# Kernel optimization log

Measured on AMD Instinct MI355X. Metric: run time of the kernel, lower is better.

Reference implementation:

```python
import jax, jax.numpy as jnp
import numpy as np

NUM_HEADS = 6
HEAD_SIZE = 64
N_EMBD = 384


def setup_inputs() -> dict:
    key = jax.random.key(0)
    ks = jax.random.split(key, 6)
    B, T, C = 4, 2048, N_EMBD
    D = NUM_HEADS * HEAD_SIZE  # 384
    x = jax.random.normal(ks[0], (B, T, C), dtype=jnp.float32)
    scale = 1.0 / np.sqrt(C)
    Wq = jax.random.normal(ks[1], (C, D), dtype=jnp.float32) * scale
    Wk = jax.random.normal(ks[2], (C, D), dtype=jnp.float32) * scale
    Wv = jax.random.normal(ks[3], (C, D), dtype=jnp.float32) * scale
    Wp = jax.random.normal(ks[4], (D, N_EMBD), dtype=jnp.float32) * scale
    bp = jnp.zeros((N_EMBD,), dtype=jnp.float32)
    return {"x": x, "Wq": Wq, "Wk": Wk, "Wv": Wv, "Wp": Wp, "bp": bp}


def reference(x, Wq, Wk, Wv, Wp, bp):
    B, T, C = x.shape
    H, Dh = NUM_HEADS, HEAD_SIZE
    # QKV projections (no bias), split into heads: [B, H, T, Dh]
    q = (x @ Wq).reshape(B, T, H, Dh).transpose(0, 2, 1, 3)
    k = (x @ Wk).reshape(B, T, H, Dh).transpose(0, 2, 1, 3)
    v = (x @ Wv).reshape(B, T, H, Dh).transpose(0, 2, 1, 3)
    # scaled dot-product scores [B, H, T, T]
    scores = jnp.einsum("bhqd,bhkd->bhqk", q, k) / jnp.sqrt(jnp.float32(Dh))
    causal = jnp.tril(jnp.ones((T, T), dtype=bool))
    scores = jnp.where(causal, scores, jnp.float32(-1e9))
    attn = jax.nn.softmax(scores, axis=-1)
    # dropout is identity at inference (Keras Dropout inactive outside training)
    out = jnp.einsum("bhqk,bhkd->bhqd", attn, v)
    out = out.transpose(0, 2, 1, 3).reshape(B, T, H * Dh)
    return out @ Wp + bp
```

## Files before the change

### kernel.cpp

```cpp
#include <hip/hip_runtime.h>
#include <hip/hip_bf16.h>

typedef __bf16 bf16x8 __attribute__((ext_vector_type(8)));
typedef float floatx4 __attribute__((ext_vector_type(4)));
typedef unsigned short us4 __attribute__((ext_vector_type(4)));
typedef unsigned short us8 __attribute__((ext_vector_type(8)));
typedef unsigned short ushort_t;

#define MFMA(a,b,c) __builtin_amdgcn_mfma_f32_16x16x32_bf16((a),(b),(c),0,0,0)


__device__ __forceinline__ ushort_t f2bf(float f){
  unsigned u = __builtin_bit_cast(unsigned, f);
  u = u + 0x7fffu + ((u>>16)&1u);
  return (ushort_t)(u>>16);
}

__device__ __forceinline__ us4 pack4(float4 a){
  us4 o;
  o[0]=f2bf(a.x); o[1]=f2bf(a.y); o[2]=f2bf(a.z); o[3]=f2bf(a.w);
  return o;
}

__device__ __forceinline__ us4 cvt4(floatx4 v){
  union { us4 s; __hip_bfloat162 h[2]; } u;
  float2 t;
  t.x=v[0]; t.y=v[1]; u.h[0]=__float22bfloat162_rn(t);
  t.x=v[2]; t.y=v[3]; u.h[1]=__float22bfloat162_rn(t);
  return u.s;
}

__global__ __launch_bounds__(256) void prep(
    const float* __restrict__ x,
    const float* __restrict__ w0, const float* __restrict__ w1,
    const float* __restrict__ w2, const float* __restrict__ w3,
    ushort_t* __restrict__ xb,
    ushort_t* __restrict__ wt_qkv, ushort_t* __restrict__ wt_p){
  __shared__ ushort_t tile[64][65];
  int bx = blockIdx.x;
  if (bx < 3072){
    int i = (bx*256 + threadIdx.x)*4;
    float4 v = *(const float4*)(x + i);
    us4 o;
    o[0]=f2bf(v.x); o[1]=f2bf(v.y); o[2]=f2bf(v.z); o[3]=f2bf(v.w);
    *(us4*)(xb + i) = o;
    return;
  }
  int t6 = bx - 3072;
  int z = t6/36, rem = t6%36, by = rem/6, bxx = rem%6;
  const float* src; ushort_t* dst;
  if      (z==0){ src=w0; dst=wt_qkv;             }
  else if (z==1){ src=w1; dst=wt_qkv + 384*384;   }
  else if (z==2){ src=w2; dst=wt_qkv + 2*384*384; }
  else          { src=w3; dst=wt_p;               }
  int r0 = by*64, c0 = bxx*64;
  int t = threadIdx.x, r = t>>2, cs = (t&3)*16;
  #pragma unroll
  for (int i=0;i<16;i++) tile[r][cs+i] = f2bf(src[(r0+r)*384 + c0+cs+i]);
  __syncthreads();
  #pragma unroll
  for (int i=0;i<16;i++) dst[(c0+r)*384 + r0+cs+i] = tile[cs+i][r];
}

__global__ __launch_bounds__(64) void qkv_gemm(
    const ushort_t* __restrict__ x, const ushort_t* __restrict__ wt,
    ushort_t* __restrict__ qb, ushort_t* __restrict__ kb, ushort_t* __restrict__ vtb){
  int lane = threadIdx.x&63, l15 = lane&15, quad = lane>>4;
  int mb = blockIdx.x*64;
  int nb = blockIdx.y*64;
  floatx4 acc[4][4];
  #pragma unroll
  for (int qs=0;qs<4;qs++)
    #pragma unroll
    for (int nt=0;nt<4;nt++) acc[qs][nt]=(floatx4){0,0,0,0};
  #pragma unroll
  for (int kt=0; kt<12; kt++){
    bf16x8 a[4], b[4];
    #pragma unroll
    for (int qs=0; qs<4; qs++)
      a[qs] = *(const bf16x8*)(x + (mb+qs*16+l15)*384 + kt*32 + quad*8);
    #pragma unroll
    for (int nt=0; nt<4; nt++)
      b[nt] = *(const bf16x8*)(wt + (nb+nt*16+l15)*384 + kt*32 + quad*8);
    #pragma unroll
    for (int qs=0; qs<4; qs++)
      #pragma unroll
      for (int nt=0; nt<4; nt++)
        acc[qs][nt] = MFMA(a[qs], b[nt], acc[qs][nt]);
  }
  int tensor = nb/384, nc = nb%384;
  if (tensor == 2){
    #pragma unroll
    for (int qs=0; qs<4; qs++){
      int rbase = mb + qs*16 + quad*4;
      int batch = rbase >> 11, rr = rbase & 2047;
      #pragma unroll
      for (int nt=0; nt<4; nt++){
        int c = nc + nt*16 + l15;
        float4 v; v.x=acc[qs][nt][0]; v.y=acc[qs][nt][1];
                  v.z=acc[qs][nt][2]; v.w=acc[qs][nt][3];
        *(us4*)(vtb + (batch*384 + c)*2048 + rr) = pack4(v);
      }
    }
  } else {
    #pragma unroll
    for (int qs=0; qs<4; qs++){
      #pragma unroll
      for (int nt=0; nt<4; nt++){
        int c = nc + nt*16 + l15;
        #pragma unroll
        for (int j=0; j<4; j++){
          int r = mb + qs*16 + quad*4 + j;
          float val = acc[qs][nt][j];
          if (tensor==0) val *= 0.18033688011112042f;
          ushort_t hv = f2bf(val);
          if (tensor==0) qb[r*384+c] = hv;
          else           kb[r*384+c] = hv;
        }
      }
    }
  }
}

__device__ __forceinline__ void subtile(
    const bf16x8 (&kf)[4][2], const bf16x8 (&vf)[4][2], bf16x8 ones,
    bf16x8 qf0, bf16x8 qf1,
    floatx4 (&o4)[4], floatx4& lsum,
    ushort_t* pwv, int qg, int kv0, bool diag, int l15, int quad){
  floatx4 s[4];
  #pragma unroll
  for (int nt=0; nt<4; nt++){
    floatx4 z = {0,0,0,0};
    z = MFMA(kf[nt][0], qf0, z);
    z = MFMA(kf[nt][1], qf1, z);
    s[nt] = z;
  }
  ushort_t* prow = pwv + l15*72;
  if (diag){
    #pragma unroll
    for (int nt=0; nt<4; nt++){
      floatx4 p;
      #pragma unroll
      for (int r=0;r<4;r++){
        int kvg = kv0 + nt*16 + quad*4 + r;
        float sv = (kvg > qg) ? -1e30f : s[nt][r];
        p[r] = exp2f(sv);
      }
      *(us4*)(prow + nt*16 + quad*4) = cvt4(p);
    }
  } else {
    #pragma unroll
    for (int nt=0; nt<4; nt++){
      floatx4 p;
      #pragma unroll
      for (int r=0;r<4;r++) p[r] = exp2f(s[nt][r]);
      *(us4*)(prow + nt*16 + quad*4) = cvt4(p);
    }
  }
  bf16x8 pa0 = *(const bf16x8*)(prow + quad*8);
  bf16x8 pa1 = *(const bf16x8*)(prow + 32 + quad*8);
  #pragma unroll
  for (int nt=0; nt<4; nt++){
    o4[nt] = MFMA(pa0, vf[nt][0], o4[nt]);
    o4[nt] = MFMA(pa1, vf[nt][1], o4[nt]);
  }
  lsum = MFMA(pa0, ones, lsum);
  lsum = MFMA(pa1, ones, lsum);
}

__global__ __launch_bounds__(256,2) void attn(
    const ushort_t* __restrict__ qb, const ushort_t* __restrict__ kb,
    const ushort_t* __restrict__ vtb, ushort_t* __restrict__ ob){
  __shared__ float smem[4608];
  int bx = blockIdx.x;
  int hb = bx % 24;
  int qi = bx / 24;
  int qt = 31 - qi;
  int h = hb % 6, b = hb / 6;
  int lane = threadIdx.x&63, w = threadIdx.x>>6, l15 = lane&15, quad = lane>>4;
  int q0 = qt*64;
  const ushort_t* qbase = qb  + b*2048*384 + h*64;
  const ushort_t* kbase = kb  + b*2048*384 + h*64;
  const ushort_t* vbase = vtb + (b*384 + h*64)*2048;

  bf16x8 qf[4][2];
  #pragma unroll
  for (int qs=0; qs<4; qs++){
    const ushort_t* qrow = qbase + (q0+qs*16+l15)*384;
    qf[qs][0] = *(const bf16x8*)(qrow + quad*8);
    qf[qs][1] = *(const bf16x8*)(qrow + 32 + quad*8);
  }
  union { us8 u; bf16x8 v; } onesu;
  #pragma unroll
  for (int i=0;i<8;i++) onesu.u[i] = 0x3F80;
  bf16x8 ones = onesu.v;

  floatx4 o[4][4];
  floatx4 lsum[4];
  #pragma unroll
  for (int qs=0;qs<4;qs++){
    lsum[qs] = (floatx4){0,0,0,0};
    #pragma unroll
    for (int i=0;i<4;i++) o[qs][i]=(floatx4){0,0,0,0};
  }

  ushort_t* pw = (ushort_t*)smem + w*1152;

  for (int kt=w; kt<=qt; kt+=4){
    int kv0 = kt*64;
    bf16x8 kf[4][2], vf[4][2];
    #pragma unroll
    for (int nt=0; nt<4; nt++){
      const ushort_t* krow = kbase + (kv0+nt*16+l15)*384;
      kf[nt][0] = *(const bf16x8*)(krow + quad*8);
      kf[nt][1] = *(const bf16x8*)(krow + 32 + quad*8);
      const ushort_t* vrow = vbase + (nt*16+l15)*2048 + kv0;
      vf[nt][0] = *(const bf16x8*)(vrow + quad*8);
      vf[nt][1] = *(const bf16x8*)(vrow + 32 + quad*8);
    }
    bool diag = (kt == qt);
    subtile(kf,vf,ones,qf[0][0],qf[0][1], o[0], lsum[0], pw, q0   +l15, kv0, diag, l15, quad);
    subtile(kf,vf,ones,qf[1][0],qf[1][1], o[1], lsum[1], pw, q0+16+l15, kv0, diag, l15, quad);
    subtile(kf,vf,ones,qf[2][0],qf[2][1], o[2], lsum[2], pw, q0+32+l15, kv0, diag, l15, quad);
    subtile(kf,vf,ones,qf[3][0],qf[3][1], o[3], lsum[3], pw, q0+48+l15, kv0, diag, l15, quad);
  }

  float* lsh = smem + 4352;
  if (l15==0){
    #pragma unroll
    for (int qs=0;qs<4;qs++)
      #pragma unroll
      for (int j=0;j<4;j++)
        lsh[w*64 + qs*16 + quad*4 + j] = lsum[qs][j];
  }

  #pragma unroll
  for (int qs=0; qs<4; qs++){
    __syncthreads();
    #pragma unroll
    for (int j=0;j<4;j++){
      int r16 = quad*4 + j;
      #pragma unroll
      for (int nt=0;nt<4;nt++)
        smem[w*1088 + r16*68 + nt*16 + l15] = o[qs][nt][j];
    }
    __syncthreads();
    #pragma unroll
    for (int jj=0;jj<4;jj++){
      int r16 = w*4 + jj;
      float l = lsh[qs*16+r16] + lsh[64+qs*16+r16]
              + lsh[128+qs*16+r16] + lsh[192+qs*16+r16];
      float acc = smem[r16*68+lane] + smem[1088 + r16*68+lane]
                + smem[2176 + r16*68+lane] + smem[3264 + r16*68+lane];
      ob[(b*2048 + q0 + qs*16 + r16)*384 + h*64 + lane] = f2bf(acc/l);
    }
  }
}

__global__ __launch_bounds__(64) void proj_gemm(
    const ushort_t* __restrict__ a, const ushort_t* __restrict__ wpt,
    const float* __restrict__ bp, float* __restrict__ out){
  int lane = threadIdx.x&63, l15 = lane&15, quad = lane>>4;
  int mb = blockIdx.x*64;
  int nb = blockIdx.y*64;
  floatx4 acc[4][4];
  #pragma unroll
  for (int qs=0;qs<4;qs++)
    #pragma unroll
    for (int nt=0;nt<4;nt++) acc[qs][nt]=(floatx4){0,0,0,0};
  #pragma unroll
  for (int kt=0; kt<12; kt++){
    bf16x8 av[4], bv[4];
    #pragma unroll
    for (int qs=0; qs<4; qs++)
      av[qs] = *(const bf16x8*)(a + (mb+qs*16+l15)*384 + kt*32 + quad*8);
    #pragma unroll
    for (int nt=0; nt<4; nt++)
      bv[nt] = *(const bf16x8*)(wpt + (nb+nt*16+l15)*384 + kt*32 + quad*8);
    #pragma unroll
    for (int qs=0; qs<4; qs++)
      #pragma unroll
      for (int nt=0; nt<4; nt++)
        acc[qs][nt] = MFMA(av[qs], bv[nt], acc[qs][nt]);
  }
  #pragma unroll
  for (int qs=0; qs<4; qs++){
    #pragma unroll
    for (int nt=0; nt<4; nt++){
      int c = nb + nt*16 + l15;
      float bias = bp[c];
      #pragma unroll
      for (int j=0; j<4; j++){
        int r = mb + qs*16 + quad*4 + j;
        out[r*384 + c] = acc[qs][nt][j] + bias;
      }
    }
  }
}

extern "C" void kernel_launch(void* const* d_in, const int* in_sizes, int n_in,
                              void* d_out, int out_size, void* d_ws, size_t ws_size,
                              hipStream_t stream){
  const float* x  = (const float*)d_in[0];
  const float* Wq = (const float*)d_in[1];
  const float* Wk = (const float*)d_in[2];
  const float* Wv = (const float*)d_in[3];
  const float* Wp = (const float*)d_in[4];
  const float* bp = (const float*)d_in[5];
  float* out = (float*)d_out;

  ushort_t* xb  = (ushort_t*)d_ws;
  ushort_t* wt  = xb  + 8192*384;
  ushort_t* wpt = wt  + 1152*384;
  ushort_t* qb  = wpt + 384*384;
  ushort_t* kb  = qb  + 8192*384;
  ushort_t* vtb = kb  + 8192*384;
  ushort_t* ab  = vtb + 8192*384;

  prep     <<<dim3(3216),   256, 0, stream>>>(x,Wq,Wk,Wv,Wp,xb,wt,wpt);
  qkv_gemm <<<dim3(128,18), 64,  0, stream>>>(xb, wt, qb, kb, vtb);
  attn     <<<dim3(768),    256, 0, stream>>>(qb, kb, vtb, ab);
  proj_gemm<<<dim3(128,6),  64,  0, stream>>>(ab, wpt, bp, out);
}
```

Measured before the change: 155.5 us.

## Store all bf16 operands in MFMA-fragment-tiled layout for contiguous loads

Every intermediate buffer (x, weights, Q, K, V^T, attention output) is rewritten in a 16-row by 8-element tiled layout, so each lane's bf16x8 fragment load makes a wavefront read contiguous 128-element chunks instead of strided rows. Producers (prep, qkv epilogue, attention epilogue) scatter into the new layout and consumers index it directly. The aim is coalesced global loads in the GEMMs and the attention inner loop. The cost is more scattered, sub-word stores in the epilogues and more complex index arithmetic.

Result: faster. 137.1 us (-11.9%).

```diff
diff --git a/kernel.cpp b/kernel.cpp
--- a/kernel.cpp
+++ b/kernel.cpp
@@ -40,34 +40,43 @@
   int bx = blockIdx.x;
   if (bx < 3072){
     int i = (bx*256 + threadIdx.x)*4;
+    int row = i/384, col = i - row*384;
     float4 v = *(const float4*)(x + i);
     us4 o;
     o[0]=f2bf(v.x); o[1]=f2bf(v.y); o[2]=f2bf(v.z); o[3]=f2bf(v.w);
-    *(us4*)(xb + i) = o;
+    *(us4*)(xb + ((row>>4)*48 + (col>>3))*128 + (row&15)*8 + (col&7)) = o;
     return;
   }
   int t6 = bx - 3072;
   int z = t6/36, rem = t6%36, by = rem/6, bxx = rem%6;
   const float* src; ushort_t* dst;
   if      (z==0){ src=w0; dst=wt_qkv;             }
-  else if (z==1){ src=w1; dst=wt_qkv + 384*384;   }
-  else if (z==2){ src=w2; dst=wt_qkv + 2*384*384; }
+  else if (z==1){ src=w1; dst=wt_qkv + 147456;    }
+  else if (z==2){ src=w2; dst=wt_qkv + 2*147456;  }
   else          { src=w3; dst=wt_p;               }
   int r0 = by*64, c0 = bxx*64;
   int t = threadIdx.x, r = t>>2, cs = (t&3)*16;
   #pragma unroll
   for (int i=0;i<16;i++) tile[r][cs+i] = f2bf(src[(r0+r)*384 + c0+cs+i]);
   __syncthreads();
-  #pragma unroll
-  for (int i=0;i<16;i++) dst[(c0+r)*384 + r0+cs+i] = tile[cs+i][r];
+  int n = c0 + r, t16n = n>>4, rn = n&15;
+  int k0 = r0 + cs;
+  #pragma unroll
+  for (int i=0;i<16;i++){
+    int k = k0 + i;
+    dst[(t16n*48 + (k>>3))*128 + rn*8 + (k&7)] = tile[cs+i][r];
+  }
 }
 
 __global__ __launch_bounds__(64) void qkv_gemm(
     const ushort_t* __restrict__ x, const ushort_t* __restrict__ wt,
     ushort_t* __restrict__ qb, ushort_t* __restrict__ kb, ushort_t* __restrict__ vtb){
   int lane = threadIdx.x&63, l15 = lane&15, quad = lane>>4;
-  int mb = blockIdx.x*64;
-  int nb = blockIdx.y*64;
+  int mb = blockIdx.x*64, mt = blockIdx.x*4;
+  int z  = blockIdx.y/6;
+  int nt16 = (blockIdx.y - z*6)*4;
+  int n0 = nt16*16;
+  const ushort_t* wbase = wt + z*147456;
   floatx4 acc[4][4];
   #pragma unroll
   for (int qs=0;qs<4;qs++)
@@ -78,44 +87,47 @@
     bf16x8 a[4], b[4];
     #pragma unroll
     for (int qs=0; qs<4; qs++)
-      a[qs] = *(const bf16x8*)(x + (mb+qs*16+l15)*384 + kt*32 + quad*8);
+      a[qs] = *(const bf16x8*)(x + ((mt+qs)*48 + kt*4+quad)*128 + l15*8);
     #pragma unroll
     for (int nt=0; nt<4; nt++)
-      b[nt] = *(const bf16x8*)(wt + (nb+nt*16+l15)*384 + kt*32 + quad*8);
+      b[nt] = *(const bf16x8*)(wbase + ((nt16+nt)*48 + kt*4+quad)*128 + l15*8);
     #pragma unroll
     for (int qs=0; qs<4; qs++)
       #pragma unroll
       for (int nt=0; nt<4; nt++)
         acc[qs][nt] = MFMA(a[qs], b[nt], acc[qs][nt]);
   }
-  int tensor = nb/384, nc = nb%384;
-  if (tensor == 2){
+  int h = n0>>6;
+  if (z == 2){
     #pragma unroll
     for (int qs=0; qs<4; qs++){
       int rbase = mb + qs*16 + quad*4;
-      int batch = rbase >> 11, rr = rbase & 2047;
+      int b_ = rbase >> 11, rr = rbase & 2047;
+      int ct = rr>>3, e0 = rr&7;
       #pragma unroll
       for (int nt=0; nt<4; nt++){
-        int c = nc + nt*16 + l15;
         float4 v; v.x=acc[qs][nt][0]; v.y=acc[qs][nt][1];
                   v.z=acc[qs][nt][2]; v.w=acc[qs][nt][3];
-        *(us4*)(vtb + (batch*384 + c)*2048 + rr) = pack4(v);
+        *(us4*)(vtb + ((b_*6+h)*1024 + nt*256 + ct)*128 + l15*8 + e0) = pack4(v);
       }
     }
   } else {
     #pragma unroll
     for (int qs=0; qs<4; qs++){
+      int rbase = mb + qs*16 + quad*4;
+      int b_ = rbase>>11, rr = rbase&2047;
+      int t16 = rr>>4, rlo = rr&15;
       #pragma unroll
       for (int nt=0; nt<4; nt++){
-        int c = nc + nt*16 + l15;
+        int hc = nt*16 + l15;
+        int base = ((b_*6+h)*1024 + t16*8 + (hc>>3))*128 + (hc&7);
         #pragma unroll
         for (int j=0; j<4; j++){
-          int r = mb + qs*16 + quad*4 + j;
           float val = acc[qs][nt][j];
-          if (tensor==0) val *= 0.18033688011112042f;
+          if (z==0) val *= 0.18033688011112042f;
           ushort_t hv = f2bf(val);
-          if (tensor==0) qb[r*384+c] = hv;
-          else           kb[r*384+c] = hv;
+          if (z==0) qb[base + (rlo+j)*8] = hv;
+          else      kb[base + (rlo+j)*8] = hv;
         }
       }
     }
@@ -179,16 +191,16 @@
   int h = hb % 6, b = hb / 6;
   int lane = threadIdx.x&63, w = threadIdx.x>>6, l15 = lane&15, quad = lane>>4;
   int q0 = qt*64;
-  const ushort_t* qbase = qb  + b*2048*384 + h*64;
-  const ushort_t* kbase = kb  + b*2048*384 + h*64;
-  const ushort_t* vbase = vtb + (b*384 + h*64)*2048;
+  const ushort_t* qbase = qb  + (b*6+h)*131072;
+  const ushort_t* kbase = kb  + (b*6+h)*131072;
+  const ushort_t* vbase = vtb + (b*6+h)*131072;
 
   bf16x8 qf[4][2];
   #pragma unroll
   for (int qs=0; qs<4; qs++){
-    const ushort_t* qrow = qbase + (q0+qs*16+l15)*384;
-    qf[qs][0] = *(const bf16x8*)(qrow + quad*8);
-    qf[qs][1] = *(const bf16x8*)(qrow + 32 + quad*8);
+    const ushort_t* qp = qbase + ((qt*4+qs)*8 + quad)*128 + l15*8;
+    qf[qs][0] = *(const bf16x8*)(qp);
+    qf[qs][1] = *(const bf16x8*)(qp + 512);
   }
   union { us8 u; bf16x8 v; } onesu;
   #pragma unroll
@@ -211,12 +223,12 @@
     bf16x8 kf[4][2], vf[4][2];
     #pragma unroll
     for (int nt=0; nt<4; nt++){
-      const ushort_t* krow = kbase + (kv0+nt*16+l15)*384;
-      kf[nt][0] = *(const bf16x8*)(krow + quad*8);
-      kf[nt][1] = *(const bf16x8*)(krow + 32 + quad*8);
-      const ushort_t* vrow = vbase + (nt*16+l15)*2048 + kv0;
-      vf[nt][0] = *(const bf16x8*)(vrow + quad*8);
-      vf[nt][1] = *(const bf16x8*)(vrow + 32 + quad*8);
+      const ushort_t* kp = kbase + ((kt*4+nt)*8 + quad)*128 + l15*8;
+      kf[nt][0] = *(const bf16x8*)(kp);
+      kf[nt][1] = *(const bf16x8*)(kp + 512);
+      const ushort_t* vp = vbase + (nt*256 + kt*8 + quad)*128 + l15*8;
+      vf[nt][0] = *(const bf16x8*)(vp);
+      vf[nt][1] = *(const bf16x8*)(vp + 512);
     }
     bool diag = (kt == qt);
     subtile(kf,vf,ones,qf[0][0],qf[0][1], o[0], lsum[0], pw, q0   +l15, kv0, diag, l15, quad);
@@ -252,7 +264,8 @@
               + lsh[128+qs*16+r16] + lsh[192+qs*16+r16];
       float acc = smem[r16*68+lane] + smem[1088 + r16*68+lane]
                 + smem[2176 + r16*68+lane] + smem[3264 + r16*68+lane];
-      ob[(b*2048 + q0 + qs*16 + r16)*384 + h*64 + lane] = f2bf(acc/l);
+      ob[((b*128 + qt*4 + qs)*48 + h*8 + (lane>>3))*128 + r16*8 + (lane&7)]
+          = f2bf(acc/l);
     }
   }
 }
@@ -261,8 +274,8 @@
     const ushort_t* __restrict__ a, const ushort_t* __restrict__ wpt,
     const float* __restrict__ bp, float* __restrict__ out){
   int lane = threadIdx.x&63, l15 = lane&15, quad = lane>>4;
-  int mb = blockIdx.x*64;
-  int nb = blockIdx.y*64;
+  int mb = blockIdx.x*64, mt = blockIdx.x*4;
+  int nb = blockIdx.y*64, nt16 = blockIdx.y*4;
   floatx4 acc[4][4];
   #pragma unroll
   for (int qs=0;qs<4;qs++)
@@ -273,10 +286,10 @@
     bf16x8 av[4], bv[4];
     #pragma unroll
     for (int qs=0; qs<4; qs++)
-      av[qs] = *(const bf16x8*)(a + (mb+qs*16+l15)*384 + kt*32 + quad*8);
+      av[qs] = *(const bf16x8*)(a + ((mt+qs)*48 + kt*4+quad)*128 + l15*8);
     #pragma unroll
     for (int nt=0; nt<4; nt++)
-      bv[nt] = *(const bf16x8*)(wpt + (nb+nt*16+l15)*384 + kt*32 + quad*8);
+      bv[nt] = *(const bf16x8*)(wpt + ((nt16+nt)*48 + kt*4+quad)*128 + l15*8);
     #pragma unroll
     for (int qs=0; qs<4; qs++)
       #pragma unroll
```
